# Optimization experiments

Measured on AMD Instinct MI355X. Metric: run time of the kernel, lower is better.

## Reference

```python
import jax, jax.numpy as jnp
import numpy as np

D_MODEL, N_HEAD, HEAD_SIZE = 1024, 16, 64
NEG_INF = -1e30


def setup_inputs() -> dict:
    key = jax.random.key(0)
    ks = jax.random.split(key, 12)
    B, S = 4, 4096
    w = 0.02
    return {
        "query": jax.random.normal(ks[0], (B, S, D_MODEL), jnp.float32),
        "key":   jax.random.normal(ks[1], (B, S, D_MODEL), jnp.float32),
        "value": jax.random.normal(ks[2], (B, S, D_MODEL), jnp.float32),
        "mask":  jnp.ones((HEAD_SIZE, HEAD_SIZE), jnp.int32),
        "Wq": jax.random.normal(ks[3], (D_MODEL, HEAD_SIZE), jnp.float32) * w,
        "bq": jnp.zeros((HEAD_SIZE,), jnp.float32),
        "Wk": jax.random.normal(ks[4], (D_MODEL, HEAD_SIZE), jnp.float32) * w,
        "bk": jnp.zeros((HEAD_SIZE,), jnp.float32),
        "Wv": jax.random.normal(ks[5], (D_MODEL, HEAD_SIZE), jnp.float32) * w,
        "bv": jnp.zeros((HEAD_SIZE,), jnp.float32),
        "Wp": jax.random.normal(ks[6], (D_MODEL, D_MODEL), jnp.float32) * w,
        "bp": jnp.zeros((D_MODEL,), jnp.float32),
    }


def reference(query, key, value, mask, Wq, bq, Wk, bk, Wv, bv, Wp, bp):
    h, dh = N_HEAD, HEAD_SIZE
    # Linear projections: (B,S,d_model) -> (B,S,head_size)
    q = query @ Wq + bq
    k = key @ Wk + bk
    v = value @ Wv + bv
    # Faithful to torch: view(-1, h, dh).transpose(1,2) on (B,S,head_size)
    # -> (N, dh, h) with N = B*S/h
    q = q.reshape(-1, h, dh).transpose(0, 2, 1)
    k = k.reshape(-1, h, dh).transpose(0, 2, 1)
    v = v.reshape(-1, h, dh).transpose(0, 2, 1)
    scale = q.shape[-1] ** (-0.5)  # dhead = h in the original code
    # scores: (N, dh, dh)
    scores = jnp.einsum('nik,njk->nij', q, k) * scale
    scores = jnp.where(mask == 0, NEG_INF, scores)
    # NOTE: original code computes softmax(scores) but then overwrites it;
    # the actual output uses dropout(raw scores) @ v. Dropout in eval = identity.
    x = jnp.einsum('nij,njh->nih', scores, v)  # (N, dh, h)
    x = x.transpose(0, 2, 1).reshape(-1, h * dh)  # (N, d_model)
    return x @ Wp + bp
```

## Files before the change

### kernel.cpp

```cpp
#include <hip/hip_runtime.h>
#include <hip/hip_bf16.h>
#include <stdint.h>


typedef float f32x4 __attribute__((ext_vector_type(4)));
typedef short s16x8 __attribute__((ext_vector_type(8)));

#define T_TOK 16384
#define KDIM  1024
#define HS    64

__device__ __forceinline__ short f2bf(float f) {
    union { float f; uint32_t u; } x; x.f = f;
    uint32_t u = x.u;
    u += 0x7FFFu + ((u >> 16) & 1u);
    return (short)(u >> 16);
}

__global__ __launch_bounds__(256) void wtrans_kernel(
    const float* __restrict__ Wq, const float* __restrict__ Wk,
    const float* __restrict__ Wv, const float* __restrict__ Wp,
    short* __restrict__ Wtq, short* __restrict__ Wtk,
    short* __restrict__ Wtv, short* __restrict__ Wpt)
{
    const int bid = blockIdx.x;
    const float* src; short* dst; int N, k0, n0;
    if (bid < 256) { src = Wp; dst = Wpt; N = 1024; k0 = (bid >> 4) * 64; n0 = (bid & 15) * 64; }
    else {
        int r = bid - 256; int p = r >> 4;
        src = (p == 0) ? Wq : (p == 1) ? Wk : Wv;
        dst = (p == 0) ? Wtq : (p == 1) ? Wtk : Wtv;
        N = 64; k0 = (r & 15) * 64; n0 = 0;
    }
    __shared__ float Ts[64][68];
    const int tid = threadIdx.x;
    #pragma unroll
    for (int i = 0; i < 4; ++i) {
        int idx = i * 256 + tid;
        int r = idx >> 4, c4 = idx & 15;
        f32x4 v = *(const f32x4*)&src[(size_t)(k0 + r) * N + n0 + c4 * 4];
        *(f32x4*)&Ts[r][c4 * 4] = v;
    }
    __syncthreads();
    #pragma unroll
    for (int i = 0; i < 2; ++i) {
        int idx = i * 256 + tid;
        int n = idx >> 3, c8 = idx & 7;
        s16x8 h;
        #pragma unroll
        for (int j = 0; j < 8; ++j) h[j] = f2bf(Ts[c8 * 8 + j][n]);
        *(s16x8*)&dst[(size_t)(n0 + n) * KDIM + k0 + c8 * 8] = h;
    }
}

__global__ __launch_bounds__(256) void qkv_proj_kernel(
    const float* __restrict__ Q, const float* __restrict__ K,
    const float* __restrict__ V,
    const short* __restrict__ Wtq, const short* __restrict__ Wtk,
    const short* __restrict__ Wtv,
    const float* __restrict__ bq, const float* __restrict__ bk,
    const float* __restrict__ bv,
    float* __restrict__ OutQKV)
{
    const int p = blockIdx.y;
    const float* In = (p == 0) ? Q : (p == 1) ? K : V;
    const short* Wt = (p == 0) ? Wtq : (p == 1) ? Wtk : Wtv;
    const float* bb = (p == 0) ? bq : (p == 1) ? bk : bv;
    float* Out = OutQKV + (size_t)p * T_TOK * HS;

    const int tid  = threadIdx.x;
    const int wave = tid >> 6;
    const int lane = tid & 63;
    const int lhi  = lane >> 4;
    const int llo  = lane & 15;
    const int t0   = blockIdx.x * 64;

    const float* Ap = In + (size_t)(t0 + wave * 16 + llo) * KDIM + lhi * 8;
    const short* Bp = Wt + (size_t)llo * KDIM + lhi * 8;

    f32x4 acc[4] = {};

    #pragma unroll
    for (int c = 0; c < 16; ++c) {
        const int k0 = c * 64;
        f32x4 a0l = *(const f32x4*)(Ap + k0);
        f32x4 a0h = *(const f32x4*)(Ap + k0 + 4);
        f32x4 a1l = *(const f32x4*)(Ap + k0 + 32);
        f32x4 a1h = *(const f32x4*)(Ap + k0 + 36);
        s16x8 bfr[2][4];
        #pragma unroll
        for (int hh = 0; hh < 2; ++hh)
            #pragma unroll
            for (int nb = 0; nb < 4; ++nb)
                bfr[hh][nb] = *(const s16x8*)(Bp + (size_t)nb * 16 * KDIM + k0 + hh * 32);
        s16x8 af0, af1;
        af0[0] = f2bf(a0l.x); af0[1] = f2bf(a0l.y); af0[2] = f2bf(a0l.z); af0[3] = f2bf(a0l.w);
        af0[4] = f2bf(a0h.x); af0[5] = f2bf(a0h.y); af0[6] = f2bf(a0h.z); af0[7] = f2bf(a0h.w);
        af1[0] = f2bf(a1l.x); af1[1] = f2bf(a1l.y); af1[2] = f2bf(a1l.z); af1[3] = f2bf(a1l.w);
        af1[4] = f2bf(a1h.x); af1[5] = f2bf(a1h.y); af1[6] = f2bf(a1h.z); af1[7] = f2bf(a1h.w);
        #pragma unroll
        for (int nb = 0; nb < 4; ++nb)
            acc[nb] = __builtin_amdgcn_mfma_f32_16x16x32_bf16(af0, bfr[0][nb], acc[nb], 0, 0, 0);
        #pragma unroll
        for (int nb = 0; nb < 4; ++nb)
            acc[nb] = __builtin_amdgcn_mfma_f32_16x16x32_bf16(af1, bfr[1][nb], acc[nb], 0, 0, 0);
    }

    #pragma unroll
    for (int nb = 0; nb < 4; ++nb) {
        const float bias = bb[nb * 16 + llo];
        #pragma unroll
        for (int r = 0; r < 4; ++r)
            Out[(size_t)(t0 + wave * 16 + lhi * 4 + r) * HS + nb * 16 + llo] = acc[nb][r] + bias;
    }
}

__global__ __launch_bounds__(256) void group_attn_kernel(
    const float* __restrict__ QKV, short* __restrict__ Xbf)
{
    const int n = blockIdx.x;
    __shared__ float Sq[16][68];
    __shared__ float Sk[16][68];
    __shared__ float Sv[16][68];
    __shared__ float KV[16][17];

    const int tid = threadIdx.x;
    const float* qp = QKV + (size_t)n * 16 * HS;
    const float* kp = qp + (size_t)T_TOK * HS;
    const float* vp = kp + (size_t)T_TOK * HS;

    {
        int row = tid >> 4, c4 = (tid & 15) * 4;
        *(f32x4*)&Sq[row][c4] = *(const f32x4*)&qp[tid * 4];
        *(f32x4*)&Sk[row][c4] = *(const f32x4*)&kp[tid * 4];
        *(f32x4*)&Sv[row][c4] = *(const f32x4*)&vp[tid * 4];
    }
    __syncthreads();

    {
        int b = tid >> 4, a = tid & 15;
        const f32x4* kb = (const f32x4*)&Sk[b][0];
        const f32x4* va = (const f32x4*)&Sv[a][0];
        float s = 0.f;
        #pragma unroll
        for (int j = 0; j < 16; ++j) {
            f32x4 x = kb[j], y = va[j];
            s += x.x * y.x + x.y * y.y + x.z * y.z + x.w * y.w;
        }
        KV[b][a] = s * 0.25f;
    }
    __syncthreads();

    const int i = tid & 63;
    const int w = tid >> 6;
    float qv[16];
    #pragma unroll
    for (int b = 0; b < 16; ++b) qv[b] = Sq[b][i];
    #pragma unroll
    for (int u = 0; u < 4; ++u) {
        int a = u * 4 + w;
        float s = 0.f;
        #pragma unroll
        for (int b = 0; b < 16; ++b) s += qv[b] * KV[b][a];
        Xbf[(size_t)n * 1024 + a * 64 + i] = f2bf(s);
    }
}

__global__ __launch_bounds__(256) void out_proj_kernel(
    const short* __restrict__ Xbf, const short* __restrict__ Wpt,
    const float* __restrict__ bp, float* __restrict__ Out)
{
    const int tid  = threadIdx.x;
    const int wave = tid >> 6;
    const int lane = tid & 63;
    const int lhi  = lane >> 4, llo = lane & 15;
    const int n0   = blockIdx.x * 64;
    const int m0   = blockIdx.y * 64;

    const short* Ap = Xbf + (size_t)(m0 + wave * 16 + llo) * KDIM + lhi * 8;
    const short* Bp = Wpt + (size_t)(n0 + llo) * KDIM + lhi * 8;

    f32x4 acc[4] = {};

    #pragma unroll
    for (int c = 0; c < 16; ++c) {
        const int k0 = c * 64;
        s16x8 af0 = *(const s16x8*)(Ap + k0);
        s16x8 af1 = *(const s16x8*)(Ap + k0 + 32);
        s16x8 bfr[2][4];
        #pragma unroll
        for (int hh = 0; hh < 2; ++hh)
            #pragma unroll
            for (int nb = 0; nb < 4; ++nb)
                bfr[hh][nb] = *(const s16x8*)(Bp + (size_t)nb * 16 * KDIM + k0 + hh * 32);
        #pragma unroll
        for (int nb = 0; nb < 4; ++nb)
            acc[nb] = __builtin_amdgcn_mfma_f32_16x16x32_bf16(af0, bfr[0][nb], acc[nb], 0, 0, 0);
        #pragma unroll
        for (int nb = 0; nb < 4; ++nb)
            acc[nb] = __builtin_amdgcn_mfma_f32_16x16x32_bf16(af1, bfr[1][nb], acc[nb], 0, 0, 0);
    }

    #pragma unroll
    for (int nb = 0; nb < 4; ++nb) {
        const float bias = bp[n0 + nb * 16 + llo];
        #pragma unroll
        for (int r = 0; r < 4; ++r)
            Out[(size_t)(m0 + wave * 16 + lhi * 4 + r) * KDIM + n0 + nb * 16 + llo]
                = acc[nb][r] + bias;
    }
}

extern "C" void kernel_launch(void* const* d_in, const int* in_sizes, int n_in,
                              void* d_out, int out_size, void* d_ws, size_t ws_size,
                              hipStream_t stream) {
    const float* Q  = (const float*)d_in[0];
    const float* K  = (const float*)d_in[1];
    const float* V  = (const float*)d_in[2];
    const float* Wq = (const float*)d_in[4];
    const float* bq = (const float*)d_in[5];
    const float* Wk = (const float*)d_in[6];
    const float* bk = (const float*)d_in[7];
    const float* Wv = (const float*)d_in[8];
    const float* bv = (const float*)d_in[9];
    const float* Wp = (const float*)d_in[10];
    const float* bp = (const float*)d_in[11];
    float* out = (float*)d_out;

    char* ws = (char*)d_ws;
    float* qkv = (float*)ws;
    size_t off = (size_t)3 * T_TOK * HS * sizeof(float);
    short* Xbf = (short*)(ws + off); off += (size_t)1024 * 1024 * 2;
    short* Wtq = (short*)(ws + off); off += (size_t)HS * KDIM * 2;
    short* Wtk = (short*)(ws + off); off += (size_t)HS * KDIM * 2;
    short* Wtv = (short*)(ws + off); off += (size_t)HS * KDIM * 2;
    short* Wpt = (short*)(ws + off); off += (size_t)KDIM * KDIM * 2;

    wtrans_kernel<<<dim3(304), 256, 0, stream>>>(Wq, Wk, Wv, Wp, Wtq, Wtk, Wtv, Wpt);
    qkv_proj_kernel<<<dim3(T_TOK / 64, 3), 256, 0, stream>>>(
        Q, K, V, Wtq, Wtk, Wtv, bq, bk, bv, qkv);
    group_attn_kernel<<<dim3(1024), 256, 0, stream>>>(qkv, Xbf);
    out_proj_kernel<<<dim3(16, 16), 256, 0, stream>>>(Xbf, Wpt, bp, out);
}
```

Baseline: 268.1 us.

## Split QKV projection K dimension across two blocks and shrink out-proj tiles

```diff
diff --git a/kernel.cpp b/kernel.cpp
--- a/kernel.cpp
+++ b/kernel.cpp
@@ -63,10 +63,11 @@
     float* __restrict__ OutQKV)
 {
     const int p = blockIdx.y;
+    const int z = blockIdx.z;
     const float* In = (p == 0) ? Q : (p == 1) ? K : V;
     const short* Wt = (p == 0) ? Wtq : (p == 1) ? Wtk : Wtv;
     const float* bb = (p == 0) ? bq : (p == 1) ? bk : bv;
-    float* Out = OutQKV + (size_t)p * T_TOK * HS;
+    float* Out = OutQKV + ((size_t)z * 3 + p) * T_TOK * HS;
 
     const int tid  = threadIdx.x;
     const int wave = tid >> 6;
@@ -74,14 +75,15 @@
     const int lhi  = lane >> 4;
     const int llo  = lane & 15;
     const int t0   = blockIdx.x * 64;
-
-    const float* Ap = In + (size_t)(t0 + wave * 16 + llo) * KDIM + lhi * 8;
-    const short* Bp = Wt + (size_t)llo * KDIM + lhi * 8;
+    const int kb   = z * 512;
+
+    const float* Ap = In + (size_t)(t0 + wave * 16 + llo) * KDIM + kb + lhi * 8;
+    const short* Bp = Wt + (size_t)llo * KDIM + kb + lhi * 8;
 
     f32x4 acc[4] = {};
 
     #pragma unroll
-    for (int c = 0; c < 16; ++c) {
+    for (int c = 0; c < 8; ++c) {
         const int k0 = c * 64;
         f32x4 a0l = *(const f32x4*)(Ap + k0);
         f32x4 a0h = *(const f32x4*)(Ap + k0 + 4);
@@ -108,7 +110,7 @@
 
     #pragma unroll
     for (int nb = 0; nb < 4; ++nb) {
-        const float bias = bb[nb * 16 + llo];
+        const float bias = (z == 0) ? bb[nb * 16 + llo] : 0.0f;
         #pragma unroll
         for (int r = 0; r < 4; ++r)
             Out[(size_t)(t0 + wave * 16 + lhi * 4 + r) * HS + nb * 16 + llo] = acc[nb][r] + bias;
@@ -125,15 +127,22 @@
     __shared__ float KV[16][17];
 
     const int tid = threadIdx.x;
+    const size_t zoff = (size_t)3 * T_TOK * HS;
     const float* qp = QKV + (size_t)n * 16 * HS;
     const float* kp = qp + (size_t)T_TOK * HS;
     const float* vp = kp + (size_t)T_TOK * HS;
 
     {
         int row = tid >> 4, c4 = (tid & 15) * 4;
-        *(f32x4*)&Sq[row][c4] = *(const f32x4*)&qp[tid * 4];
-        *(f32x4*)&Sk[row][c4] = *(const f32x4*)&kp[tid * 4];
-        *(f32x4*)&Sv[row][c4] = *(const f32x4*)&vp[tid * 4];
+        f32x4 q0 = *(const f32x4*)&qp[tid * 4];
+        f32x4 q1 = *(const f32x4*)&qp[zoff + tid * 4];
+        f32x4 k0 = *(const f32x4*)&kp[tid * 4];
+        f32x4 k1 = *(const f32x4*)&kp[zoff + tid * 4];
+        f32x4 v0 = *(const f32x4*)&vp[tid * 4];
+        f32x4 v1 = *(const f32x4*)&vp[zoff + tid * 4];
+        *(f32x4*)&Sq[row][c4] = q0 + q1;
+        *(f32x4*)&Sk[row][c4] = k0 + k1;
+        *(f32x4*)&Sv[row][c4] = v0 + v1;
     }
     __syncthreads();
 
@@ -174,41 +183,29 @@
     const int wave = tid >> 6;
     const int lane = tid & 63;
     const int lhi  = lane >> 4, llo = lane & 15;
-    const int n0   = blockIdx.x * 64;
-    const int m0   = blockIdx.y * 64;
-
-    const short* Ap = Xbf + (size_t)(m0 + wave * 16 + llo) * KDIM + lhi * 8;
+    const int n0   = blockIdx.x * 32 + (wave & 1) * 16;
+    const int m0   = blockIdx.y * 32 + (wave >> 1) * 16;
+
+    const short* Ap = Xbf + (size_t)(m0 + llo) * KDIM + lhi * 8;
     const short* Bp = Wpt + (size_t)(n0 + llo) * KDIM + lhi * 8;
 
-    f32x4 acc[4] = {};
+    f32x4 acc = {};
 
     #pragma unroll
     for (int c = 0; c < 16; ++c) {
         const int k0 = c * 64;
         s16x8 af0 = *(const s16x8*)(Ap + k0);
         s16x8 af1 = *(const s16x8*)(Ap + k0 + 32);
-        s16x8 bfr[2][4];
-        #pragma unroll
-        for (int hh = 0; hh < 2; ++hh)
-            #pragma unroll
-            for (int nb = 0; nb < 4; ++nb)
-                bfr[hh][nb] = *(const s16x8*)(Bp + (size_t)nb * 16 * KDIM + k0 + hh * 32);
-        #pragma unroll
-        for (int nb = 0; nb < 4; ++nb)
-            acc[nb] = __builtin_amdgcn_mfma_f32_16x16x32_bf16(af0, bfr[0][nb], acc[nb], 0, 0, 0);
-        #pragma unroll
-        for (int nb = 0; nb < 4; ++nb)
-            acc[nb] = __builtin_amdgcn_mfma_f32_16x16x32_bf16(af1, bfr[1][nb], acc[nb], 0, 0, 0);
-    }
-
-    #pragma unroll
-    for (int nb = 0; nb < 4; ++nb) {
-        const float bias = bp[n0 + nb * 16 + llo];
-        #pragma unroll
-        for (int r = 0; r < 4; ++r)
-            Out[(size_t)(m0 + wave * 16 + lhi * 4 + r) * KDIM + n0 + nb * 16 + llo]
-                = acc[nb][r] + bias;
-    }
+        s16x8 bf0 = *(const s16x8*)(Bp + k0);
+        s16x8 bf1 = *(const s16x8*)(Bp + k0 + 32);
+        acc = __builtin_amdgcn_mfma_f32_16x16x32_bf16(af0, bf0, acc, 0, 0, 0);
+        acc = __builtin_amdgcn_mfma_f32_16x16x32_bf16(af1, bf1, acc, 0, 0, 0);
+    }
+
+    const float bias = bp[n0 + llo];
+    #pragma unroll
+    for (int r = 0; r < 4; ++r)
+        Out[(size_t)(m0 + lhi * 4 + r) * KDIM + n0 + llo] = acc[r] + bias;
 }
 
 extern "C" void kernel_launch(void* const* d_in, const int* in_sizes, int n_in,
@@ -229,7 +226,7 @@
 
     char* ws = (char*)d_ws;
     float* qkv = (float*)ws;
-    size_t off = (size_t)3 * T_TOK * HS * sizeof(float);
+    size_t off = (size_t)2 * 3 * T_TOK * HS * sizeof(float);
     short* Xbf = (short*)(ws + off); off += (size_t)1024 * 1024 * 2;
     short* Wtq = (short*)(ws + off); off += (size_t)HS * KDIM * 2;
     short* Wtk = (short*)(ws + off); off += (size_t)HS * KDIM * 2;
@@ -237,8 +234,8 @@
     short* Wpt = (short*)(ws + off); off += (size_t)KDIM * KDIM * 2;
 
     wtrans_kernel<<<dim3(304), 256, 0, stream>>>(Wq, Wk, Wv, Wp, Wtq, Wtk, Wtv, Wpt);
-    qkv_proj_kernel<<<dim3(T_TOK / 64, 3), 256, 0, stream>>>(
+    qkv_proj_kernel<<<dim3(T_TOK / 64, 3, 2), 256, 0, stream>>>(
         Q, K, V, Wtq, Wtk, Wtv, bq, bk, bv, qkv);
     group_attn_kernel<<<dim3(1024), 256, 0, stream>>>(qkv, Xbf);
-    out_proj_kernel<<<dim3(16, 16), 256, 0, stream>>>(Xbf, Wpt, bp, out);
-}
+    out_proj_kernel<<<dim3(32, 32), 256, 0, stream>>>(Xbf, Wpt, bp, out);
+}
```

After: 281.3 us. 4.9% more time.
